# Kernel optimization log

Hardware: AMD Instinct MI355X
Metric: run time of the kernel (lower is better)

The kernel has to match this reference:

```python
import jax, jax.numpy as jnp
import numpy as np

B, L, C_IN, C_HID, C_HH, C_OUT = 512, 512, 32, 64, 128, 10


def setup_inputs() -> dict:
    key = jax.random.key(0)
    ks = jax.random.split(key, 12)
    shp = (B, L - 1, C_IN)
    return {
        "times": jnp.arange(L, dtype=jnp.float32),
        "coeff_a": 0.1 * jax.random.normal(ks[0], shp, jnp.float32),
        "coeff_b": 0.1 * jax.random.normal(ks[1], shp, jnp.float32),
        "coeff_two_c": 0.1 * jax.random.normal(ks[2], shp, jnp.float32),
        "coeff_three_d": 0.1 * jax.random.normal(ks[3], shp, jnp.float32),
        "final_index": jax.random.randint(ks[4], (B,), 0, L, jnp.int64 if jax.config.jax_enable_x64 else jnp.int32),
        # params (init scale ~ 1/sqrt(fan_in))
        "W_init": jax.random.normal(ks[5], (C_IN, C_HID), jnp.float32) / np.sqrt(C_IN),
        "b_init": jnp.zeros((C_HID,), jnp.float32),
        "W1": jax.random.normal(ks[6], (C_HID + C_IN, C_HH), jnp.float32) / np.sqrt(C_HID + C_IN),
        "b1": jnp.zeros((C_HH,), jnp.float32),
        "W2": jax.random.normal(ks[7], (C_HH, C_HID), jnp.float32) / np.sqrt(C_HH),
        "b2": jnp.zeros((C_HID,), jnp.float32),
        "W_out": jax.random.normal(ks[8], (C_HID, C_OUT), jnp.float32) / np.sqrt(C_HID),
        "b_out": jnp.zeros((C_OUT,), jnp.float32),
    }


def _spline_eval(t, times, a, b, two_c, three_d):
    # Natural cubic spline evaluation (controldiffeq.NaturalCubicSpline.evaluate)
    # coeffs: [B, L-1, C]; t scalar -> [B, C]
    maxi = a.shape[1] - 1
    idx = jnp.clip(jnp.searchsorted(times, t, side="right") - 1, 0, maxi)
    frac = t - times[idx]
    inner = 0.5 * two_c[:, idx] + three_d[:, idx] * (frac / 3.0)
    inner = b[:, idx] + inner * frac
    return a[:, idx] + inner * frac


def reference(times, coeff_a, coeff_b, coeff_two_c, coeff_three_d, final_index,
              W_init, b_init, W1, b1, W2, b2, W_out, b_out):
    def X(t):
        return _spline_eval(t, times, coeff_a, coeff_b, coeff_two_c, coeff_three_d)

    def f(t, z):  # vector field: func(z, X(t))
        h = jnp.tanh(jnp.concatenate([z, X(t)], axis=-1) @ W1 + b1)
        return jnp.tanh(h @ W2 + b2)

    # torchdiffeq fixed-step 'rk4' uses the 3/8 rule (rk4_alt_step_func);
    # step_size = min(diff(times)) == grid spacing here, so steps land on `times`.
    def step(z, tdt):
        t, dt = tdt
        k1 = f(t, z)
        k2 = f(t + dt / 3.0, z + dt * k1 / 3.0)
        k3 = f(t + 2.0 * dt / 3.0, z + dt * (k2 - k1 / 3.0))
        k4 = f(t + dt, z + dt * (k1 - k2 + k3))
        z_new = z + dt * (k1 + 3.0 * (k2 + k3) + k4) / 8.0
        return z_new, z_new

    z0 = X(times[0]) @ W_init + b_init  # [B, H]
    dts = times[1:] - times[:-1]
    _, zs = jax.lax.scan(step, z0, (times[:-1], dts))
    z_all = jnp.concatenate([z0[None], zs], axis=0)  # [L, B, H]
    # gather per-batch final time (equivalent to the unique/gather logic in forward)
    z_T = z_all[final_index, jnp.arange(z_all.shape[1])]  # [B, H]
    return z_T @ W_out + b_out  # [B, C_OUT]
```

## Files before the change

kernel.cpp:

```cpp
#include <hip/hip_runtime.h>
#include <hip/hip_bf16.h>

#define NSEQ 512
#define SEGS 511
#define CIN  32

typedef float v2f __attribute__((ext_vector_type(2)));
typedef float v4f __attribute__((ext_vector_type(4)));

__device__ __forceinline__ float rl(float v, int lane) {
    return __int_as_float(__builtin_amdgcn_readlane(__float_as_int(v), lane));
}

__device__ __forceinline__ float tanhf_fast(float x) {
    float ax = fabsf(x);
    float e = __expf(-2.0f * ax);
#if __has_builtin(__builtin_amdgcn_rcpf)
    float r = (1.0f - e) * __builtin_amdgcn_rcpf(1.0f + e);
#else
    float r = (1.0f - e) / (1.0f + e);
#endif
    return copysignf(r, x);
}

__device__ __forceinline__ void pkfma(v2f& acc, v2f a, v2f b) {
    asm("v_pk_fma_f32 %0, %1, %2, %0" : "+v"(acc) : "v"(a), "v"(b));
}

__attribute__((amdgpu_waves_per_eu(1, 1)))
__global__ __launch_bounds__(128) void node_kernel(
    const float* __restrict__ cA, const float* __restrict__ cB,
    const float* __restrict__ cC, const float* __restrict__ cD,
    const int*   __restrict__ final_index,
    const float* __restrict__ W_init, const float* __restrict__ b_init,
    const float* __restrict__ W1, const float* __restrict__ b1,
    const float* __restrict__ W2, const float* __restrict__ b2,
    const float* __restrict__ W_out, const float* __restrict__ b_out,
    float* __restrict__ out)
{
    __shared__ __align__(16) float ysb[2][2][64];
    __shared__ __align__(16) float xvb[2][4][32];
    __shared__ __align__(16) float hb [2][2][64];
    __shared__ float zz[2][2][64];

    const int tid  = threadIdx.x;
    const int lane = tid & 63;
    const int w    = tid >> 6;
    const int b    = blockIdx.x;
    const int ch   = lane & 31;
    const int col  = 64 * w + lane;

    v2f w1p[48];
#pragma unroll
    for (int i = 0; i < 48; ++i) {
        w1p[i].x = W1[(2 * i) * 128 + col];
        w1p[i].y = W1[(2 * i + 1) * 128 + col];
    }
    v2f w2p[32];
#pragma unroll
    for (int i = 0; i < 32; ++i) {
        w2p[i].x = W2[(64 * w + 2 * i) * 64 + lane];
        w2p[i].y = W2[(64 * w + 2 * i + 1) * 64 + lane];
    }
    float b1c = b1[col];
    float b2m = b2[lane];

#pragma unroll
    for (int i = 0; i < 48; ++i) asm volatile("" : "+v"(w1p[i]));
#pragma unroll
    for (int i = 0; i < 32; ++i) asm volatile("" : "+v"(w2p[i]));
    asm volatile("" : "+v"(b1c));
    asm volatile("" : "+v"(b2m));

    const float* a_ptr = cA + (size_t)b * SEGS * CIN;
    const float* bp    = cB + (size_t)b * SEGS * CIN;
    const float* cp    = cC + (size_t)b * SEGS * CIN;
    const float* dp    = cD + (size_t)b * SEGS * CIN;

    float z = b_init[lane];
    {
        float a0 = a_ptr[ch];
#pragma unroll
        for (int i = 0; i < 32; ++i)
            z = fmaf(rl(a0, i), W_init[i * 64 + lane], z);
    }

    const int fi = final_index[b];

    float acur = a_ptr[ch], bcur = bp[ch], ccur = cp[ch], dcur = dp[ch];
    float k1 = 0.f, k2 = 0.f, k3 = 0.f, k4 = 0.f;

    __syncthreads();

#define MM_STAGE(YSV, XS, PAR, KOUT) do {                                    \
    ysb[PAR][w][lane] = (YSV);                                               \
    v2f accA = {0.f, 0.f}, accB = {0.f, 0.f};                                \
    _Pragma("unroll")                                                        \
    for (int q = 0; q < 16; ++q) {                                           \
        v4f u = *reinterpret_cast<const v4f*>(&ysb[PAR][w][4 * q]);          \
        v2f u01 = __builtin_shufflevector(u, u, 0, 1);                       \
        v2f u23 = __builtin_shufflevector(u, u, 2, 3);                       \
        pkfma(accA, u01, w1p[2 * q]);                                        \
        pkfma(accB, u23, w1p[2 * q + 1]);                                    \
    }                                                                        \
    _Pragma("unroll")                                                        \
    for (int q = 0; q < 8; ++q) {                                            \
        v4f u = *reinterpret_cast<const v4f*>(&xvb[w][XS][4 * q]);           \
        v2f u01 = __builtin_shufflevector(u, u, 0, 1);                       \
        v2f u23 = __builtin_shufflevector(u, u, 2, 3);                       \
        pkfma(accA, u01, w1p[32 + 2 * q]);                                   \
        pkfma(accB, u23, w1p[33 + 2 * q]);                                   \
    }                                                                        \
    float h = tanhf_fast((accA.x + accB.x) + (accA.y + accB.y) + b1c);       \
    hb[PAR][w][lane] = h;                                                    \
    v2f za = {0.f, 0.f}, zb = {0.f, 0.f};                                    \
    _Pragma("unroll")                                                        \
    for (int q = 0; q < 16; ++q) {                                           \
        v4f hv = *reinterpret_cast<const v4f*>(&hb[PAR][w][4 * q]);          \
        v2f h01 = __builtin_shufflevector(hv, hv, 0, 1);                     \
        v2f h23 = __builtin_shufflevector(hv, hv, 2, 3);                     \
        pkfma(za, h01, w2p[2 * q]);                                          \
        pkfma(zb, h23, w2p[2 * q + 1]);                                      \
    }                                                                        \
    float zw = (za.x + zb.x) + (za.y + zb.y);                                \
    zz[PAR][w][lane] = zw;                                                   \
    __syncthreads();                                                         \
    float zo = zz[PAR][w ^ 1][lane];                                         \
    KOUT = tanhf_fast(zw + zo + b2m);                                        \
} while (0)

    for (int t = 0; t < fi; ++t) {
        float i13 = fmaf(dcur, 1.0f / 9.0f, 0.5f * ccur);
        float x13 = fmaf(fmaf(i13, 1.0f / 3.0f, bcur), 1.0f / 3.0f, acur);
        float i23 = fmaf(dcur, 2.0f / 9.0f, 0.5f * ccur);
        float x23 = fmaf(fmaf(i23, 2.0f / 3.0f, bcur), 2.0f / 3.0f, acur);
        float xbl = acur + (bcur + (0.5f * ccur + dcur * (1.0f / 3.0f)));
        xvb[w][0][ch] = acur;
        xvb[w][1][ch] = x13;
        xvb[w][2][ch] = x23;

        const int tn  = (t + 1 < SEGS) ? (t + 1) : (SEGS - 1);
        const int off = tn * CIN + ch;
        float anx = a_ptr[off];
        float bnx = bp[off];
        float cnx = cp[off];
        float dnx = dp[off];

        MM_STAGE(z, 0, 0, k1);
        float xb = (t < SEGS - 1) ? anx : xbl;
        xvb[w][3][ch] = xb;
        float ys1 = fmaf(k1, 1.0f / 3.0f, z);
        MM_STAGE(ys1, 1, 1, k2);
        float ys2 = z + (k2 - k1 * (1.0f / 3.0f));
        MM_STAGE(ys2, 2, 0, k3);
        float ys3 = z + (k1 - k2 + k3);
        MM_STAGE(ys3, 3, 1, k4);

        z += (k1 + 3.0f * (k2 + k3) + k4) * 0.125f;
        acur = anx; bcur = bnx; ccur = cnx; dcur = dnx;
    }

    if (w == 0 && lane < 10) {
        float acc = b_out[lane];
#pragma unroll
        for (int m = 0; m < 64; ++m)
            acc = fmaf(rl(z, m), W_out[m * 10 + lane], acc);
        out[b * 10 + lane] = acc;
    }
}

extern "C" void kernel_launch(void* const* d_in, const int* in_sizes, int n_in,
                              void* d_out, int out_size, void* d_ws, size_t ws_size,
                              hipStream_t stream) {
    const float* cA     = (const float*)d_in[1];
    const float* cBc    = (const float*)d_in[2];
    const float* cCc    = (const float*)d_in[3];
    const float* cDc    = (const float*)d_in[4];
    const int*   fidx   = (const int*)d_in[5];
    const float* W_init = (const float*)d_in[6];
    const float* b_init = (const float*)d_in[7];
    const float* W1     = (const float*)d_in[8];
    const float* b1     = (const float*)d_in[9];
    const float* W2     = (const float*)d_in[10];
    const float* b2     = (const float*)d_in[11];
    const float* W_out  = (const float*)d_in[12];
    const float* b_out  = (const float*)d_in[13];

    node_kernel<<<dim3(NSEQ), dim3(128), 0, stream>>>(
        cA, cBc, cCc, cDc, fidx, W_init, b_init, W1, b1, W2, b2, W_out, b_out,
        (float*)d_out);
}
```

Before: 1.373 ms.

## Split W1 matmul by linearity so input projections leave the RK4 stage chain

Uses the linearity of the first layer to split each RK stage's pre-activation into a z@W1z term, the spline-input projections X@W1x for all four stage times, and k@W1z corrections built from earlier stage outputs. The z and X dot products are computed once per step, independent of the stage chain. Each serial stage therefore only needs a 64-wide dot instead of a 96-wide one, shortening the latency-bound dependency chain. Total FLOPs stay the same, and floating-point summation order changes slightly.

Result: no change. 1.370 ms (-0.3%).

```diff
diff --git a/kernel.cpp b/kernel.cpp
--- a/kernel.cpp
+++ b/kernel.cpp
@@ -38,9 +38,10 @@
     const float* __restrict__ W_out, const float* __restrict__ b_out,
     float* __restrict__ out)
 {
-    __shared__ __align__(16) float ysb[2][2][64];
-    __shared__ __align__(16) float xvb[2][4][32];
-    __shared__ __align__(16) float hb [2][2][64];
+    __shared__ __align__(16) float zbc [2][64];
+    __shared__ __align__(16) float xvb [2][4][32];
+    __shared__ __align__(16) float kbc [2][2][64];
+    __shared__ __align__(16) float hbuf[2][2][64];
     __shared__ float zz[2][2][64];
 
     const int tid  = threadIdx.x;
@@ -50,11 +51,17 @@
     const int ch   = lane & 31;
     const int col  = 64 * w + lane;
 
-    v2f w1p[48];
-#pragma unroll
-    for (int i = 0; i < 48; ++i) {
-        w1p[i].x = W1[(2 * i) * 128 + col];
-        w1p[i].y = W1[(2 * i + 1) * 128 + col];
+    v2f w1z[32];
+#pragma unroll
+    for (int i = 0; i < 32; ++i) {
+        w1z[i].x = W1[(2 * i) * 128 + col];
+        w1z[i].y = W1[(2 * i + 1) * 128 + col];
+    }
+    v2f w1x[16];
+#pragma unroll
+    for (int i = 0; i < 16; ++i) {
+        w1x[i].x = W1[(64 + 2 * i) * 128 + col];
+        w1x[i].y = W1[(65 + 2 * i) * 128 + col];
     }
     v2f w2p[32];
 #pragma unroll
@@ -66,7 +73,9 @@
     float b2m = b2[lane];
 
 #pragma unroll
-    for (int i = 0; i < 48; ++i) asm volatile("" : "+v"(w1p[i]));
+    for (int i = 0; i < 32; ++i) asm volatile("" : "+v"(w1z[i]));
+#pragma unroll
+    for (int i = 0; i < 16; ++i) asm volatile("" : "+v"(w1x[i]));
 #pragma unroll
     for (int i = 0; i < 32; ++i) asm volatile("" : "+v"(w2p[i]));
     asm volatile("" : "+v"(b1c));
@@ -88,48 +97,56 @@
     const int fi = final_index[b];
 
     float acur = a_ptr[ch], bcur = bp[ch], ccur = cp[ch], dcur = dp[ch];
-    float k1 = 0.f, k2 = 0.f, k3 = 0.f, k4 = 0.f;
 
     __syncthreads();
 
-#define MM_STAGE(YSV, XS, PAR, KOUT) do {                                    \
-    ysb[PAR][w][lane] = (YSV);                                               \
-    v2f accA = {0.f, 0.f}, accB = {0.f, 0.f};                                \
+#define DOT64(BUF, WP, OUT) do {                                             \
+    v2f dA = {0.f, 0.f}, dB = {0.f, 0.f};                                    \
     _Pragma("unroll")                                                        \
     for (int q = 0; q < 16; ++q) {                                           \
-        v4f u = *reinterpret_cast<const v4f*>(&ysb[PAR][w][4 * q]);          \
+        v4f u = *reinterpret_cast<const v4f*>(&(BUF)[4 * q]);                \
         v2f u01 = __builtin_shufflevector(u, u, 0, 1);                       \
         v2f u23 = __builtin_shufflevector(u, u, 2, 3);                       \
-        pkfma(accA, u01, w1p[2 * q]);                                        \
-        pkfma(accB, u23, w1p[2 * q + 1]);                                    \
+        pkfma(dA, u01, (WP)[2 * q]);                                         \
+        pkfma(dB, u23, (WP)[2 * q + 1]);                                     \
     }                                                                        \
+    OUT = (dA.x + dB.x) + (dA.y + dB.y);                                     \
+} while (0)
+
+#define DOT32(BUF, WP, OUT) do {                                             \
+    v2f dA = {0.f, 0.f}, dB = {0.f, 0.f};                                    \
     _Pragma("unroll")                                                        \
     for (int q = 0; q < 8; ++q) {                                            \
-        v4f u = *reinterpret_cast<const v4f*>(&xvb[w][XS][4 * q]);           \
+        v4f u = *reinterpret_cast<const v4f*>(&(BUF)[4 * q]);                \
         v2f u01 = __builtin_shufflevector(u, u, 0, 1);                       \
         v2f u23 = __builtin_shufflevector(u, u, 2, 3);                       \
-        pkfma(accA, u01, w1p[32 + 2 * q]);                                   \
-        pkfma(accB, u23, w1p[33 + 2 * q]);                                   \
+        pkfma(dA, u01, (WP)[2 * q]);                                         \
+        pkfma(dB, u23, (WP)[2 * q + 1]);                                     \
     }                                                                        \
-    float h = tanhf_fast((accA.x + accB.x) + (accA.y + accB.y) + b1c);       \
-    hb[PAR][w][lane] = h;                                                    \
-    v2f za = {0.f, 0.f}, zb = {0.f, 0.f};                                    \
+    OUT = (dA.x + dB.x) + (dA.y + dB.y);                                     \
+} while (0)
+
+#define STAGE(ARG, PAR, KOUT) do {                                           \
+    float h = tanhf_fast(ARG);                                               \
+    hbuf[w][PAR][lane] = h;                                                  \
+    v2f za = {0.f, 0.f}, zb2 = {0.f, 0.f};                                   \
     _Pragma("unroll")                                                        \
     for (int q = 0; q < 16; ++q) {                                           \
-        v4f hv = *reinterpret_cast<const v4f*>(&hb[PAR][w][4 * q]);          \
+        v4f hv = *reinterpret_cast<const v4f*>(&hbuf[w][PAR][4 * q]);        \
         v2f h01 = __builtin_shufflevector(hv, hv, 0, 1);                     \
         v2f h23 = __builtin_shufflevector(hv, hv, 2, 3);                     \
         pkfma(za, h01, w2p[2 * q]);                                          \
-        pkfma(zb, h23, w2p[2 * q + 1]);                                      \
+        pkfma(zb2, h23, w2p[2 * q + 1]);                                     \
     }                                                                        \
-    float zw = (za.x + zb.x) + (za.y + zb.y);                                \
+    float zw = (za.x + zb2.x) + (za.y + zb2.y);                              \
     zz[PAR][w][lane] = zw;                                                   \
     __syncthreads();                                                         \
-    float zo = zz[PAR][w ^ 1][lane];                                         \
-    KOUT = tanhf_fast(zw + zo + b2m);                                        \
+    float z3 = zw + zz[PAR][w ^ 1][lane] + b2m;                              \
+    KOUT = tanhf_fast(z3);                                                   \
 } while (0)
 
     for (int t = 0; t < fi; ++t) {
+        zbc[w][lane] = z;
         float i13 = fmaf(dcur, 1.0f / 9.0f, 0.5f * ccur);
         float x13 = fmaf(fmaf(i13, 1.0f / 3.0f, bcur), 1.0f / 3.0f, acur);
         float i23 = fmaf(dcur, 2.0f / 9.0f, 0.5f * ccur);
@@ -146,15 +163,42 @@
         float cnx = cp[off];
         float dnx = dp[off];
 
-        MM_STAGE(z, 0, 0, k1);
+        float Zs;
+        DOT64(zbc[w], w1z, Zs);
+        Zs += b1c;
+        float XP0, XP1, XP2;
+        DOT32(xvb[w][0], w1x, XP0);
+        DOT32(xvb[w][1], w1x, XP1);
+        DOT32(xvb[w][2], w1x, XP2);
+        float hb0 = Zs + XP0, hb1 = Zs + XP1, hb2 = Zs + XP2;
+
+        float k1;
+        STAGE(hb0, 0, k1);
+        kbc[w][0][lane] = k1;
+
         float xb = (t < SEGS - 1) ? anx : xbl;
         xvb[w][3][ch] = xb;
-        float ys1 = fmaf(k1, 1.0f / 3.0f, z);
-        MM_STAGE(ys1, 1, 1, k2);
-        float ys2 = z + (k2 - k1 * (1.0f / 3.0f));
-        MM_STAGE(ys2, 2, 0, k3);
-        float ys3 = z + (k1 - k2 + k3);
-        MM_STAGE(ys3, 3, 1, k4);
+        float XP3;
+        DOT32(xvb[w][3], w1x, XP3);
+        float hb3 = Zs + XP3;
+
+        float K1;
+        DOT64(kbc[w][0], w1z, K1);
+
+        float k2;
+        STAGE(fmaf(K1, 1.0f / 3.0f, hb1), 1, k2);
+        kbc[w][1][lane] = k2;
+        float K2;
+        DOT64(kbc[w][1], w1z, K2);
+
+        float k3;
+        STAGE(hb2 + (K2 - K1 * (1.0f / 3.0f)), 0, k3);
+        kbc[w][0][lane] = k3;
+        float K3;
+        DOT64(kbc[w][0], w1z, K3);
+
+        float k4;
+        STAGE(hb3 + ((K1 - K2) + K3), 1, k4);
 
         z += (k1 + 3.0f * (k2 + k3) + k4) * 0.125f;
         acur = anx; bcur = bnx; ccur = cnx; dcur = dnx;
```
